# Optimization experiments

Hardware: AMD Instinct MI355X
Metric: run time of the kernel (lower is better)

The kernel has to match this reference:

```python
import jax, jax.numpy as jnp
import numpy as np

B, M, T, L, K = 64, 16, 2048, 64, 32
N = T - L + 1  # 1985 sliding-window positions


def setup_inputs() -> dict:
    key = jax.random.key(0)
    k1, k2, k3 = jax.random.split(key, 3)
    x = jax.random.normal(k1, (B, M, T), dtype=jnp.float32)
    # shapelets initialized uniform(-1, 1) as in nn.init.uniform_
    shapelets = jax.random.uniform(k2, (K, L), dtype=jnp.float32, minval=-1.0, maxval=1.0)
    # penalty maps (learned; zeros at init, random here for a non-trivial weighting)
    penalty_maps = 0.1 * jax.random.normal(k3, (K, M, N), dtype=jnp.float32)
    return {"x": x, "shapelets": shapelets, "penalty_maps": penalty_maps}


def reference(x, shapelets, penalty_maps):
    # x: (B, M, T); shapelets: (K, L); penalty_maps: (K, M, N)
    Lw = shapelets.shape[1]
    n_pos = x.shape[2] - Lw + 1
    # sliding-window view: (B, M, N, L), equivalent to torch unfold(dim=2, size=L, step=1)
    idx = jnp.arange(n_pos)[:, None] + jnp.arange(Lw)[None, :]
    sub = x[:, :, idx]  # (B, M, N, L)

    def per_shapelet(args):
        shp, pmap = args  # (L,), (M, N)
        # raw squared L2 distance over window, per channel/position: (B, M, N)
        raw = jnp.sum((sub - shp[None, None, None, :]) ** 2, axis=3)
        pen = jax.nn.elu(-pmap) + 2.0  # (M, N)
        wd = jnp.sum(raw * pen[None], axis=1)  # sum over channels -> (B, N)
        return jnp.min(wd, axis=1)  # min over positions -> (B,)

    # sequential map over the K shapelets avoids a Kx blow-up of the (B,M,N,L) intermediate
    feats = jax.lax.map(per_shapelet, (shapelets, penalty_maps))  # (K, B)
    return feats.T  # (B, K)
```

## Files before the change

kernel.cpp:

```cpp
#include <hip/hip_runtime.h>
#include <hip/hip_bf16.h>

#define B_ 64
#define M_ 16
#define T_ 2048
#define L_ 64
#define K_ 32
#define N_ (T_ - L_ + 1)
#define TN 64
#define NB 2
#define NTH 256
#define XROW 128
#define STSTR 72
#define SQSTR 68

typedef __attribute__((ext_vector_type(8))) short bf16x8;
typedef __attribute__((ext_vector_type(4))) float f32x4;

__device__ __forceinline__ unsigned short f2bf(float f) {
    __hip_bfloat16 h = __float2bfloat16(f);
    return __builtin_bit_cast(unsigned short, h);
}

__device__ __forceinline__ unsigned funnel16(unsigned lo, unsigned hi, unsigned sh) {
    return (unsigned)(((((unsigned long long)hi) << 32) | lo) >> sh);
}

__device__ __forceinline__ bf16x8 extract_frag(uint4 a, uint4 b, unsigned sh, int c2) {
    unsigned t0 = funnel16(a.x, a.y, sh), t1 = funnel16(a.y, a.z, sh);
    unsigned t2 = funnel16(a.z, a.w, sh), t3 = funnel16(a.w, b.x, sh);
    unsigned t4 = funnel16(b.x, b.y, sh), t5 = funnel16(b.y, b.z, sh);
    unsigned t6 = funnel16(b.z, b.w, sh);
    const bool s2 = (c2 & 2), s1 = (c2 & 1);
    unsigned u0 = s2 ? t2 : t0, u1 = s2 ? t3 : t1, u2 = s2 ? t4 : t2;
    unsigned u3 = s2 ? t5 : t3, u4 = s2 ? t6 : t4;
    union { unsigned u[4]; bf16x8 v; } cvt;
    cvt.u[0] = s1 ? u1 : u0; cvt.u[1] = s1 ? u2 : u1;
    cvt.u[2] = s1 ? u3 : u2; cvt.u[3] = s1 ? u4 : u3;
    return cvt.v;
}

__global__ void init_out_kernel(unsigned* __restrict__ out) {
    int i = blockIdx.x * 256 + threadIdx.x;
    if (i < B_ * K_) out[i] = 0x7F800000u;
}

__global__ __launch_bounds__(NTH, 2)
void shapelet_mfma_kernel(const float* __restrict__ x,
                          const float* __restrict__ shp,
                          const float* __restrict__ pmap,
                          unsigned* __restrict__ out) {
    __shared__ __align__(16) unsigned short xbuf[NB][M_][XROW];
    __shared__ __align__(16) unsigned short st[K_][STSTR];
    __shared__ __align__(16) float sqw[NB][M_][SQSTR];
    __shared__ float ss_l[K_];

    const int tid = threadIdx.x;
    const int n0 = blockIdx.x * TN;
    const int b0 = blockIdx.y * NB;
    const bool fast = (n0 + TN < T_);

    for (int g = tid; g < NB * M_ * 32; g += NTH) {
        const int bi = g >> 9, m = (g >> 5) & 15, j4 = (g & 31) * 4;
        const float* src = x + ((size_t)(b0 + bi) * M_ + m) * T_ + n0 + j4;
        float4 v;
        if (fast) {
            v = *(const float4*)src;
        } else {
            v = make_float4(0.f, 0.f, 0.f, 0.f);
            const int t = n0 + j4;
            if (t     < T_) v.x = src[0];
            if (t + 1 < T_) v.y = src[1];
            if (t + 2 < T_) v.z = src[2];
            if (t + 3 < T_) v.w = src[3];
        }
        ushort4 sv = { f2bf(v.x), f2bf(v.y), f2bf(v.z), f2bf(v.w) };
        *(ushort4*)&xbuf[bi][m][j4] = sv;
    }
    for (int i = tid; i < K_ * 16; i += NTH) {
        const int k = i >> 4, l4 = (i & 15) * 4;
        float4 v = *(const float4*)(shp + k * L_ + l4);
        ushort4 sv = { f2bf(v.x), f2bf(v.y), f2bf(v.z), f2bf(v.w) };
        *(ushort4*)&st[k][l4] = sv;
    }
    if (tid < K_) {
        float s = 0.f;
        for (int l = 0; l < L_; ++l) { float v = shp[tid * L_ + l]; s = fmaf(v, v, s); }
        ss_l[tid] = s;
    }
    {
        const int pm = tid >> 3, th = tid & 7;
        const int bi = pm >> 4, m = pm & 15, j0 = th * 8;
        const float* xr = x + ((size_t)(b0 + bi) * M_ + m) * T_ + n0;
        float s = 0.f;
        if (fast) {
#pragma unroll
            for (int qd = 0; qd < 16; ++qd) {
                float4 v = *(const float4*)(xr + j0 + qd * 4);
                s = fmaf(v.x, v.x, s); s = fmaf(v.y, v.y, s);
                s = fmaf(v.z, v.z, s); s = fmaf(v.w, v.w, s);
            }
            sqw[bi][m][j0] = s;
#pragma unroll
            for (int d = 1; d < 8; ++d) {
                float a = xr[j0 + d + L_ - 1], r = xr[j0 + d - 1];
                s += a * a - r * r;
                sqw[bi][m][j0 + d] = s;
            }
        } else {
            for (int l = 0; l < L_; ++l) {
                float v = (n0 + j0 + l < T_) ? xr[j0 + l] : 0.f;
                s = fmaf(v, v, s);
            }
            sqw[bi][m][j0] = s;
            for (int d = 1; d < 8; ++d) {
                float a = (n0 + j0 + d + L_ - 1 < T_) ? xr[j0 + d + L_ - 1] : 0.f;
                float r = (n0 + j0 + d - 1 < T_) ? xr[j0 + d - 1] : 0.f;
                s += a * a - r * r;
                sqw[bi][m][j0 + d] = s;
            }
        }
    }
    __syncthreads();

    const int lane = tid & 63;
    const int w  = tid >> 6;
    const int rl = lane & 15;
    const int q  = lane >> 4;
    const int rho = rl & 7, r8 = rl >> 3;
    const unsigned sh = (unsigned)((rho & 1) * 16);
    const int c2 = rho >> 1;
    const int Gb = 2 * w + q + r8;

    bf16x8 bfr[2][2];
#pragma unroll
    for (int t = 0; t < 2; ++t)
#pragma unroll
        for (int h = 0; h < 2; ++h)
            bfr[t][h] = *(const bf16x8*)&st[16 * t + rl][8 * q + 32 * h];

    const float ssk0 = ss_l[rl], ssk1 = ss_l[16 + rl];

    f32x4 wd[NB][2];
#pragma unroll
    for (int bi = 0; bi < NB; ++bi) { wd[bi][0] = (f32x4)0.f; wd[bi][1] = (f32x4)0.f; }

    const int nrow = n0 + 16 * w + 4 * q;
    const f32x4 zero = (f32x4)0.f;

#pragma unroll 1
    for (int m = 0; m < M_; ++m) {
        float4 p0, p1;
        const float* pr0 = pmap + ((size_t)(rl * M_ + m)) * N_ + nrow;
        const float* pr1 = pmap + ((size_t)((16 + rl) * M_ + m)) * N_ + nrow;
        if (fast) {
            p0 = *(const float4*)pr0;
            p1 = *(const float4*)pr1;
        } else {
            p0 = make_float4(0.f, 0.f, 0.f, 0.f);
            p1 = make_float4(0.f, 0.f, 0.f, 0.f);
            if (nrow     < N_) { p0.x = pr0[0]; p1.x = pr1[0]; }
            if (nrow + 1 < N_) { p0.y = pr0[1]; p1.y = pr1[1]; }
            if (nrow + 2 < N_) { p0.z = pr0[2]; p1.z = pr1[2]; }
            if (nrow + 3 < N_) { p0.w = pr0[3]; p1.w = pr1[3]; }
        }
        float pen0[4], pen1[4];
        pen0[0] = (p0.x < 0.f) ? (2.f - p0.x) : (__expf(-p0.x) + 1.f);
        pen0[1] = (p0.y < 0.f) ? (2.f - p0.y) : (__expf(-p0.y) + 1.f);
        pen0[2] = (p0.z < 0.f) ? (2.f - p0.z) : (__expf(-p0.z) + 1.f);
        pen0[3] = (p0.w < 0.f) ? (2.f - p0.w) : (__expf(-p0.w) + 1.f);
        pen1[0] = (p1.x < 0.f) ? (2.f - p1.x) : (__expf(-p1.x) + 1.f);
        pen1[1] = (p1.y < 0.f) ? (2.f - p1.y) : (__expf(-p1.y) + 1.f);
        pen1[2] = (p1.z < 0.f) ? (2.f - p1.z) : (__expf(-p1.z) + 1.f);
        pen1[3] = (p1.w < 0.f) ? (2.f - p1.w) : (__expf(-p1.w) + 1.f);

#pragma unroll
        for (int bi = 0; bi < NB; ++bi) {
            const uint4* px = (const uint4*)&xbuf[bi][m][0];
            uint4 w0 = px[Gb],     w1 = px[Gb + 1];
            uint4 w2 = px[Gb + 4], w3 = px[Gb + 5];
            bf16x8 a0 = extract_frag(w0, w1, sh, c2);
            bf16x8 a1 = extract_frag(w2, w3, sh, c2);

            f32x4 corr0 = __builtin_amdgcn_mfma_f32_16x16x32_bf16(a0, bfr[0][0], zero, 0, 0, 0);
            corr0       = __builtin_amdgcn_mfma_f32_16x16x32_bf16(a1, bfr[0][1], corr0, 0, 0, 0);
            f32x4 corr1 = __builtin_amdgcn_mfma_f32_16x16x32_bf16(a0, bfr[1][0], zero, 0, 0, 0);
            corr1       = __builtin_amdgcn_mfma_f32_16x16x32_bf16(a1, bfr[1][1], corr1, 0, 0, 0);

            f32x4 sq = *(const f32x4*)&sqw[bi][m][16 * w + 4 * q];
#pragma unroll
            for (int r = 0; r < 4; ++r) {
                float t0v = fmaf(-2.f, corr0[r], sq[r] + ssk0);
                wd[bi][0][r] = fmaf(pen0[r], t0v, wd[bi][0][r]);
                float t1v = fmaf(-2.f, corr1[r], sq[r] + ssk1);
                wd[bi][1][r] = fmaf(pen1[r], t1v, wd[bi][1][r]);
            }
        }
    }

#pragma unroll
    for (int bi = 0; bi < NB; ++bi) {
#pragma unroll
        for (int t = 0; t < 2; ++t) {
            float lmin = __int_as_float(0x7F800000);
#pragma unroll
            for (int r = 0; r < 4; ++r) {
                if (nrow + r < N_) lmin = fminf(lmin, wd[bi][t][r]);
            }
            lmin = fminf(lmin, __shfl_xor(lmin, 16));
            lmin = fminf(lmin, __shfl_xor(lmin, 32));
            if (q == 0) {
                atomicMin(out + (size_t)(b0 + bi) * K_ + 16 * t + rl,
                          __float_as_uint(fmaxf(lmin, 0.f)));
            }
        }
    }
}

extern "C" void kernel_launch(void* const* d_in, const int* in_sizes, int n_in,
                              void* d_out, int out_size, void* d_ws, size_t ws_size,
                              hipStream_t stream) {
    const float* x    = (const float*)d_in[0];
    const float* shp  = (const float*)d_in[1];
    const float* pmap = (const float*)d_in[2];
    unsigned* out = (unsigned*)d_out;

    init_out_kernel<<<dim3((B_ * K_ + 255) / 256), dim3(256), 0, stream>>>(out);

    dim3 grid((N_ + TN - 1) / TN, B_ / NB);
    shapelet_mfma_kernel<<<grid, dim3(NTH), 0, stream>>>(x, shp, pmap, out);
}
```

Measured before the change: 110.6 us.

## Precompute penalty map in a prepass and process one batch per block

```diff
diff --git a/kernel.cpp b/kernel.cpp
--- a/kernel.cpp
+++ b/kernel.cpp
@@ -7,8 +7,8 @@
 #define L_ 64
 #define K_ 32
 #define N_ (T_ - L_ + 1)
+#define KMN (K_ * M_ * N_)
 #define TN 64
-#define NB 2
 #define NTH 256
 #define XROW 128
 #define STSTR 72
@@ -40,29 +40,42 @@
     return cvt.v;
 }
 
-__global__ void init_out_kernel(unsigned* __restrict__ out) {
-    int i = blockIdx.x * 256 + threadIdx.x;
-    if (i < B_ * K_) out[i] = 0x7F800000u;
+__global__ void pen_init_kernel(const float* __restrict__ pmap,
+                                float* __restrict__ pen,
+                                unsigned* __restrict__ out) {
+    const int gid = blockIdx.x * 256 + threadIdx.x;
+    if (gid < B_ * K_) out[gid] = 0x7F800000u;
+    if (gid < KMN / 4) {
+        const int i4 = gid * 4;
+        float4 p = *(const float4*)(pmap + i4);
+        float4 r;
+        r.x = (p.x < 0.f) ? (2.f - p.x) : (__expf(-p.x) + 1.f);
+        r.y = (p.y < 0.f) ? (2.f - p.y) : (__expf(-p.y) + 1.f);
+        r.z = (p.z < 0.f) ? (2.f - p.z) : (__expf(-p.z) + 1.f);
+        r.w = (p.w < 0.f) ? (2.f - p.w) : (__expf(-p.w) + 1.f);
+        *(float4*)(pen + i4) = r;
+    }
 }
 
 __global__ __launch_bounds__(NTH, 2)
 void shapelet_mfma_kernel(const float* __restrict__ x,
                           const float* __restrict__ shp,
-                          const float* __restrict__ pmap,
+                          const float* __restrict__ pen,
                           unsigned* __restrict__ out) {
-    __shared__ __align__(16) unsigned short xbuf[NB][M_][XROW];
+    __shared__ __align__(16) unsigned short xbuf[M_][XROW];
     __shared__ __align__(16) unsigned short st[K_][STSTR];
-    __shared__ __align__(16) float sqw[NB][M_][SQSTR];
+    __shared__ __align__(16) float sqw[M_][SQSTR];
     __shared__ float ss_l[K_];
 
     const int tid = threadIdx.x;
     const int n0 = blockIdx.x * TN;
-    const int b0 = blockIdx.y * NB;
+    const int b  = blockIdx.y;
     const bool fast = (n0 + TN < T_);
 
-    for (int g = tid; g < NB * M_ * 32; g += NTH) {
-        const int bi = g >> 9, m = (g >> 5) & 15, j4 = (g & 31) * 4;
-        const float* src = x + ((size_t)(b0 + bi) * M_ + m) * T_ + n0 + j4;
+    const float* xb = x + ((size_t)b * M_) * T_ + n0;
+    for (int g = tid; g < M_ * 32; g += NTH) {
+        const int m = g >> 5, j4 = (g & 31) * 4;
+        const float* src = xb + m * T_ + j4;
         float4 v;
         if (fast) {
             v = *(const float4*)src;
@@ -75,7 +88,7 @@
             if (t + 3 < T_) v.w = src[3];
         }
         ushort4 sv = { f2bf(v.x), f2bf(v.y), f2bf(v.z), f2bf(v.w) };
-        *(ushort4*)&xbuf[bi][m][j4] = sv;
+        *(ushort4*)&xbuf[m][j4] = sv;
     }
     for (int i = tid; i < K_ * 16; i += NTH) {
         const int k = i >> 4, l4 = (i & 15) * 4;
@@ -88,10 +101,9 @@
         for (int l = 0; l < L_; ++l) { float v = shp[tid * L_ + l]; s = fmaf(v, v, s); }
         ss_l[tid] = s;
     }
-    {
-        const int pm = tid >> 3, th = tid & 7;
-        const int bi = pm >> 4, m = pm & 15, j0 = th * 8;
-        const float* xr = x + ((size_t)(b0 + bi) * M_ + m) * T_ + n0;
+    if (tid < M_ * 8) {
+        const int m = tid >> 3, j0 = (tid & 7) * 8;
+        const float* xr = x + ((size_t)b * M_ + m) * T_ + n0;
         float s = 0.f;
         if (fast) {
 #pragma unroll
@@ -100,24 +112,24 @@
                 s = fmaf(v.x, v.x, s); s = fmaf(v.y, v.y, s);
                 s = fmaf(v.z, v.z, s); s = fmaf(v.w, v.w, s);
             }
-            sqw[bi][m][j0] = s;
+            sqw[m][j0] = s;
 #pragma unroll
             for (int d = 1; d < 8; ++d) {
                 float a = xr[j0 + d + L_ - 1], r = xr[j0 + d - 1];
                 s += a * a - r * r;
-                sqw[bi][m][j0 + d] = s;
+                sqw[m][j0 + d] = s;
             }
         } else {
             for (int l = 0; l < L_; ++l) {
                 float v = (n0 + j0 + l < T_) ? xr[j0 + l] : 0.f;
                 s = fmaf(v, v, s);
             }
-            sqw[bi][m][j0] = s;
+            sqw[m][j0] = s;
             for (int d = 1; d < 8; ++d) {
                 float a = (n0 + j0 + d + L_ - 1 < T_) ? xr[j0 + d + L_ - 1] : 0.f;
                 float r = (n0 + j0 + d - 1 < T_) ? xr[j0 + d - 1] : 0.f;
                 s += a * a - r * r;
-                sqw[bi][m][j0 + d] = s;
+                sqw[m][j0 + d] = s;
             }
         }
     }
@@ -141,78 +153,63 @@
 
     const float ssk0 = ss_l[rl], ssk1 = ss_l[16 + rl];
 
-    f32x4 wd[NB][2];
-#pragma unroll
-    for (int bi = 0; bi < NB; ++bi) { wd[bi][0] = (f32x4)0.f; wd[bi][1] = (f32x4)0.f; }
-
+    f32x4 wd0 = (f32x4)0.f, wd1 = (f32x4)0.f;
     const int nrow = n0 + 16 * w + 4 * q;
     const f32x4 zero = (f32x4)0.f;
 
-#pragma unroll 1
+#pragma unroll 2
     for (int m = 0; m < M_; ++m) {
         float4 p0, p1;
-        const float* pr0 = pmap + ((size_t)(rl * M_ + m)) * N_ + nrow;
-        const float* pr1 = pmap + ((size_t)((16 + rl) * M_ + m)) * N_ + nrow;
+        const float* pr0 = pen + ((size_t)(rl * M_ + m)) * N_ + nrow;
+        const float* pr1 = pen + ((size_t)((16 + rl) * M_ + m)) * N_ + nrow;
         if (fast) {
             p0 = *(const float4*)pr0;
             p1 = *(const float4*)pr1;
         } else {
-            p0 = make_float4(0.f, 0.f, 0.f, 0.f);
-            p1 = make_float4(0.f, 0.f, 0.f, 0.f);
+            p0 = make_float4(2.f, 2.f, 2.f, 2.f);
+            p1 = make_float4(2.f, 2.f, 2.f, 2.f);
             if (nrow     < N_) { p0.x = pr0[0]; p1.x = pr1[0]; }
             if (nrow + 1 < N_) { p0.y = pr0[1]; p1.y = pr1[1]; }
             if (nrow + 2 < N_) { p0.z = pr0[2]; p1.z = pr1[2]; }
             if (nrow + 3 < N_) { p0.w = pr0[3]; p1.w = pr1[3]; }
         }
-        float pen0[4], pen1[4];
-        pen0[0] = (p0.x < 0.f) ? (2.f - p0.x) : (__expf(-p0.x) + 1.f);
-        pen0[1] = (p0.y < 0.f) ? (2.f - p0.y) : (__expf(-p0.y) + 1.f);
-        pen0[2] = (p0.z < 0.f) ? (2.f - p0.z) : (__expf(-p0.z) + 1.f);
-        pen0[3] = (p0.w < 0.f) ? (2.f - p0.w) : (__expf(-p0.w) + 1.f);
-        pen1[0] = (p1.x < 0.f) ? (2.f - p1.x) : (__expf(-p1.x) + 1.f);
-        pen1[1] = (p1.y < 0.f) ? (2.f - p1.y) : (__expf(-p1.y) + 1.f);
-        pen1[2] = (p1.z < 0.f) ? (2.f - p1.z) : (__expf(-p1.z) + 1.f);
-        pen1[3] = (p1.w < 0.f) ? (2.f - p1.w) : (__expf(-p1.w) + 1.f);
-
-#pragma unroll
-        for (int bi = 0; bi < NB; ++bi) {
-            const uint4* px = (const uint4*)&xbuf[bi][m][0];
-            uint4 w0 = px[Gb],     w1 = px[Gb + 1];
-            uint4 w2 = px[Gb + 4], w3 = px[Gb + 5];
-            bf16x8 a0 = extract_frag(w0, w1, sh, c2);
-            bf16x8 a1 = extract_frag(w2, w3, sh, c2);
-
-            f32x4 corr0 = __builtin_amdgcn_mfma_f32_16x16x32_bf16(a0, bfr[0][0], zero, 0, 0, 0);
-            corr0       = __builtin_amdgcn_mfma_f32_16x16x32_bf16(a1, bfr[0][1], corr0, 0, 0, 0);
-            f32x4 corr1 = __builtin_amdgcn_mfma_f32_16x16x32_bf16(a0, bfr[1][0], zero, 0, 0, 0);
-            corr1       = __builtin_amdgcn_mfma_f32_16x16x32_bf16(a1, bfr[1][1], corr1, 0, 0, 0);
-
-            f32x4 sq = *(const f32x4*)&sqw[bi][m][16 * w + 4 * q];
-#pragma unroll
-            for (int r = 0; r < 4; ++r) {
-                float t0v = fmaf(-2.f, corr0[r], sq[r] + ssk0);
-                wd[bi][0][r] = fmaf(pen0[r], t0v, wd[bi][0][r]);
-                float t1v = fmaf(-2.f, corr1[r], sq[r] + ssk1);
-                wd[bi][1][r] = fmaf(pen1[r], t1v, wd[bi][1][r]);
-            }
-        }
-    }
-
-#pragma unroll
-    for (int bi = 0; bi < NB; ++bi) {
-#pragma unroll
-        for (int t = 0; t < 2; ++t) {
-            float lmin = __int_as_float(0x7F800000);
-#pragma unroll
-            for (int r = 0; r < 4; ++r) {
-                if (nrow + r < N_) lmin = fminf(lmin, wd[bi][t][r]);
-            }
-            lmin = fminf(lmin, __shfl_xor(lmin, 16));
-            lmin = fminf(lmin, __shfl_xor(lmin, 32));
-            if (q == 0) {
-                atomicMin(out + (size_t)(b0 + bi) * K_ + 16 * t + rl,
-                          __float_as_uint(fmaxf(lmin, 0.f)));
-            }
+
+        const uint4* px = (const uint4*)&xbuf[m][0];
+        uint4 w0 = px[Gb],     w1 = px[Gb + 1];
+        uint4 w2 = px[Gb + 4], w3 = px[Gb + 5];
+        bf16x8 a0 = extract_frag(w0, w1, sh, c2);
+        bf16x8 a1 = extract_frag(w2, w3, sh, c2);
+
+        f32x4 corr0 = __builtin_amdgcn_mfma_f32_16x16x32_bf16(a0, bfr[0][0], zero, 0, 0, 0);
+        corr0       = __builtin_amdgcn_mfma_f32_16x16x32_bf16(a1, bfr[0][1], corr0, 0, 0, 0);
+        f32x4 corr1 = __builtin_amdgcn_mfma_f32_16x16x32_bf16(a0, bfr[1][0], zero, 0, 0, 0);
+        corr1       = __builtin_amdgcn_mfma_f32_16x16x32_bf16(a1, bfr[1][1], corr1, 0, 0, 0);
+
+        f32x4 sq = *(const f32x4*)&sqw[m][16 * w + 4 * q];
+        const float pe0[4] = { p0.x, p0.y, p0.z, p0.w };
+        const float pe1[4] = { p1.x, p1.y, p1.z, p1.w };
+#pragma unroll
+        for (int r = 0; r < 4; ++r) {
+            float t0v = fmaf(-2.f, corr0[r], sq[r] + ssk0);
+            wd0[r] = fmaf(pe0[r], t0v, wd0[r]);
+            float t1v = fmaf(-2.f, corr1[r], sq[r] + ssk1);
+            wd1[r] = fmaf(pe1[r], t1v, wd1[r]);
+        }
+    }
+
+#pragma unroll
+    for (int t = 0; t < 2; ++t) {
+        float lmin = __int_as_float(0x7F800000);
+        const f32x4& wdv = t ? wd1 : wd0;
+#pragma unroll
+        for (int r = 0; r < 4; ++r) {
+            if (nrow + r < N_) lmin = fminf(lmin, wdv[r]);
+        }
+        lmin = fminf(lmin, __shfl_xor(lmin, 16));
+        lmin = fminf(lmin, __shfl_xor(lmin, 32));
+        if (q == 0) {
+            atomicMin(out + (size_t)b * K_ + 16 * t + rl,
+                      __float_as_uint(fmaxf(lmin, 0.f)));
         }
     }
 }
@@ -224,9 +221,10 @@
     const float* shp  = (const float*)d_in[1];
     const float* pmap = (const float*)d_in[2];
     unsigned* out = (unsigned*)d_out;
-
-    init_out_kernel<<<dim3((B_ * K_ + 255) / 256), dim3(256), 0, stream>>>(out);
-
-    dim3 grid((N_ + TN - 1) / TN, B_ / NB);
-    shapelet_mfma_kernel<<<grid, dim3(NTH), 0, stream>>>(x, shp, pmap, out);
-}
+    float* pen = (float*)d_ws;
+
+    pen_init_kernel<<<dim3((KMN / 4 + 255) / 256), dim3(256), 0, stream>>>(pmap, pen, out);
+
+    dim3 grid((N_ + TN - 1) / TN, B_);
+    shapelet_mfma_kernel<<<grid, dim3(NTH), 0, stream>>>(x, shp, pen, out);
+}
```

Result: faster. 106.0 us (-4.2%).

## Precompute penalty maps as fp16 in a prepass and halve position tile

Applied to the files above, without the earlier changes.

```diff
diff --git a/kernel.cpp b/kernel.cpp
--- a/kernel.cpp
+++ b/kernel.cpp
@@ -1,4 +1,5 @@
 #include <hip/hip_runtime.h>
+#include <hip/hip_fp16.h>
 #include <hip/hip_bf16.h>
 
 #define B_ 64
@@ -7,12 +8,13 @@
 #define L_ 64
 #define K_ 32
 #define N_ (T_ - L_ + 1)
-#define TN 64
+#define NP 1988
+#define TN 32
 #define NB 2
 #define NTH 256
-#define XROW 128
+#define XROW 96
 #define STSTR 72
-#define SQSTR 68
+#define SQSTR 36
 
 typedef __attribute__((ext_vector_type(8))) short bf16x8;
 typedef __attribute__((ext_vector_type(4))) float f32x4;
@@ -20,6 +22,9 @@
 __device__ __forceinline__ unsigned short f2bf(float f) {
     __hip_bfloat16 h = __float2bfloat16(f);
     return __builtin_bit_cast(unsigned short, h);
+}
+__device__ __forceinline__ float h2f(unsigned short u) {
+    return __half2float(__builtin_bit_cast(__half, u));
 }
 
 __device__ __forceinline__ unsigned funnel16(unsigned lo, unsigned hi, unsigned sh) {
@@ -40,28 +45,54 @@
     return cvt.v;
 }
 
-__global__ void init_out_kernel(unsigned* __restrict__ out) {
-    int i = blockIdx.x * 256 + threadIdx.x;
-    if (i < B_ * K_) out[i] = 0x7F800000u;
+__global__ void pen_init_kernel(const float* __restrict__ pmap,
+                                const float* __restrict__ shp,
+                                unsigned short* __restrict__ penh,
+                                float* __restrict__ ss_ws,
+                                unsigned* __restrict__ out) {
+    const int gid = blockIdx.x * 256 + threadIdx.x;
+    if (gid < B_ * K_) out[gid] = 0x7F800000u;
+    if (gid < K_) {
+        float s = 0.f;
+        for (int l = 0; l < L_; ++l) { float v = shp[gid * L_ + l]; s = fmaf(v, v, s); }
+        ss_ws[gid] = s;
+    }
+    const int RQ = NP / 4;
+    if (gid < K_ * M_ * RQ) {
+        const int r = gid / RQ;
+        const int q4 = (gid - r * RQ) * 4;
+        const float* src = pmap + (size_t)r * N_;
+        ushort4 o;
+        unsigned short* po = (unsigned short*)&o;
+#pragma unroll
+        for (int i = 0; i < 4; ++i) {
+            int n = q4 + i; if (n >= N_) n = N_ - 1;
+            const float p = src[n];
+            const float pe = (p < 0.f) ? (2.f - p) : (__expf(-p) + 1.f);
+            po[i] = __builtin_bit_cast(unsigned short, __float2half(pe));
+        }
+        *(ushort4*)(penh + (size_t)r * NP + q4) = o;
+    }
 }
 
 __global__ __launch_bounds__(NTH, 2)
 void shapelet_mfma_kernel(const float* __restrict__ x,
                           const float* __restrict__ shp,
-                          const float* __restrict__ pmap,
+                          const unsigned short* __restrict__ penh,
+                          const float* __restrict__ ss_ws,
                           unsigned* __restrict__ out) {
     __shared__ __align__(16) unsigned short xbuf[NB][M_][XROW];
     __shared__ __align__(16) unsigned short st[K_][STSTR];
     __shared__ __align__(16) float sqw[NB][M_][SQSTR];
-    __shared__ float ss_l[K_];
 
     const int tid = threadIdx.x;
     const int n0 = blockIdx.x * TN;
     const int b0 = blockIdx.y * NB;
-    const bool fast = (n0 + TN < T_);
-
-    for (int g = tid; g < NB * M_ * 32; g += NTH) {
-        const int bi = g >> 9, m = (g >> 5) & 15, j4 = (g & 31) * 4;
+    const bool fast = (n0 + XROW <= T_);
+
+    for (int g = tid; g < NB * M_ * 24; g += NTH) {
+        const int bi = g / 384, rem = g - bi * 384;
+        const int m = rem / 24, j4 = (rem - m * 24) * 4;
         const float* src = x + ((size_t)(b0 + bi) * M_ + m) * T_ + n0 + j4;
         float4 v;
         if (fast) {
@@ -83,14 +114,8 @@
         ushort4 sv = { f2bf(v.x), f2bf(v.y), f2bf(v.z), f2bf(v.w) };
         *(ushort4*)&st[k][l4] = sv;
     }
-    if (tid < K_) {
-        float s = 0.f;
-        for (int l = 0; l < L_; ++l) { float v = shp[tid * L_ + l]; s = fmaf(v, v, s); }
-        ss_l[tid] = s;
-    }
-    {
-        const int pm = tid >> 3, th = tid & 7;
-        const int bi = pm >> 4, m = pm & 15, j0 = th * 8;
+    if (tid < NB * M_ * 4) {
+        const int bi = tid >> 6, m = (tid >> 2) & 15, j0 = (tid & 3) * 8;
         const float* xr = x + ((size_t)(b0 + bi) * M_ + m) * T_ + n0;
         float s = 0.f;
         if (fast) {
@@ -124,13 +149,16 @@
     __syncthreads();
 
     const int lane = tid & 63;
-    const int w  = tid >> 6;
+    const int w    = tid >> 6;
+    const int bi   = w >> 1;
+    const int nsub = w & 1;
     const int rl = lane & 15;
     const int q  = lane >> 4;
     const int rho = rl & 7, r8 = rl >> 3;
     const unsigned sh = (unsigned)((rho & 1) * 16);
     const int c2 = rho >> 1;
-    const int Gb = 2 * w + q + r8;
+    const int Gb = 2 * nsub + q + r8;
+    const int nrow = n0 + 16 * nsub + 4 * q;
 
     bf16x8 bfr[2][2];
 #pragma unroll
@@ -139,80 +167,67 @@
         for (int h = 0; h < 2; ++h)
             bfr[t][h] = *(const bf16x8*)&st[16 * t + rl][8 * q + 32 * h];
 
-    const float ssk0 = ss_l[rl], ssk1 = ss_l[16 + rl];
-
-    f32x4 wd[NB][2];
-#pragma unroll
-    for (int bi = 0; bi < NB; ++bi) { wd[bi][0] = (f32x4)0.f; wd[bi][1] = (f32x4)0.f; }
-
-    const int nrow = n0 + 16 * w + 4 * q;
+    const float ssk0 = ss_ws[rl], ssk1 = ss_ws[16 + rl];
+
+    const unsigned short* ph0 = penh + (size_t)rl * (M_ * NP) + nrow;
+    const unsigned short* ph1 = ph0 + (size_t)16 * M_ * NP;
+
+    f32x4 wd0 = (f32x4)0.f, wd1 = (f32x4)0.f;
     const f32x4 zero = (f32x4)0.f;
 
-#pragma unroll 1
+#pragma unroll 2
     for (int m = 0; m < M_; ++m) {
-        float4 p0, p1;
-        const float* pr0 = pmap + ((size_t)(rl * M_ + m)) * N_ + nrow;
-        const float* pr1 = pmap + ((size_t)((16 + rl) * M_ + m)) * N_ + nrow;
+        float pe0[4], pe1[4];
         if (fast) {
-            p0 = *(const float4*)pr0;
-            p1 = *(const float4*)pr1;
+            ushort4 h0 = *(const ushort4*)(ph0 + (size_t)m * NP);
+            ushort4 h1 = *(const ushort4*)(ph1 + (size_t)m * NP);
+            pe0[0] = h2f(h0.x); pe0[1] = h2f(h0.y); pe0[2] = h2f(h0.z); pe0[3] = h2f(h0.w);
+            pe1[0] = h2f(h1.x); pe1[1] = h2f(h1.y); pe1[2] = h2f(h1.z); pe1[3] = h2f(h1.w);
         } else {
-            p0 = make_float4(0.f, 0.f, 0.f, 0.f);
-            p1 = make_float4(0.f, 0.f, 0.f, 0.f);
-            if (nrow     < N_) { p0.x = pr0[0]; p1.x = pr1[0]; }
-            if (nrow + 1 < N_) { p0.y = pr0[1]; p1.y = pr1[1]; }
-            if (nrow + 2 < N_) { p0.z = pr0[2]; p1.z = pr1[2]; }
-            if (nrow + 3 < N_) { p0.w = pr0[3]; p1.w = pr1[3]; }
-        }
-        float pen0[4], pen1[4];
-        pen0[0] = (p0.x < 0.f) ? (2.f - p0.x) : (__expf(-p0.x) + 1.f);
-        pen0[1] = (p0.y < 0.f) ? (2.f - p0.y) : (__expf(-p0.y) + 1.f);
-        pen0[2] = (p0.z < 0.f) ? (2.f - p0.z) : (__expf(-p0.z) + 1.f);
-        pen0[3] = (p0.w < 0.f) ? (2.f - p0.w) : (__expf(-p0.w) + 1.f);
-        pen1[0] = (p1.x < 0.f) ? (2.f - p1.x) : (__expf(-p1.x) + 1.f);
-        pen1[1] = (p1.y < 0.f) ? (2.f - p1.y) : (__expf(-p1.y) + 1.f);
-        pen1[2] = (p1.z < 0.f) ? (2.f - p1.z) : (__expf(-p1.z) + 1.f);
-        pen1[3] = (p1.w < 0.f) ? (2.f - p1.w) : (__expf(-p1.w) + 1.f);
-
-#pragma unroll
-        for (int bi = 0; bi < NB; ++bi) {
-            const uint4* px = (const uint4*)&xbuf[bi][m][0];
-            uint4 w0 = px[Gb],     w1 = px[Gb + 1];
-            uint4 w2 = px[Gb + 4], w3 = px[Gb + 5];
-            bf16x8 a0 = extract_frag(w0, w1, sh, c2);
-            bf16x8 a1 = extract_frag(w2, w3, sh, c2);
-
-            f32x4 corr0 = __builtin_amdgcn_mfma_f32_16x16x32_bf16(a0, bfr[0][0], zero, 0, 0, 0);
-            corr0       = __builtin_amdgcn_mfma_f32_16x16x32_bf16(a1, bfr[0][1], corr0, 0, 0, 0);
-            f32x4 corr1 = __builtin_amdgcn_mfma_f32_16x16x32_bf16(a0, bfr[1][0], zero, 0, 0, 0);
-            corr1       = __builtin_amdgcn_mfma_f32_16x16x32_bf16(a1, bfr[1][1], corr1, 0, 0, 0);
-
-            f32x4 sq = *(const f32x4*)&sqw[bi][m][16 * w + 4 * q];
-#pragma unroll
-            for (int r = 0; r < 4; ++r) {
-                float t0v = fmaf(-2.f, corr0[r], sq[r] + ssk0);
-                wd[bi][0][r] = fmaf(pen0[r], t0v, wd[bi][0][r]);
-                float t1v = fmaf(-2.f, corr1[r], sq[r] + ssk1);
-                wd[bi][1][r] = fmaf(pen1[r], t1v, wd[bi][1][r]);
-            }
-        }
-    }
-
-#pragma unroll
-    for (int bi = 0; bi < NB; ++bi) {
-#pragma unroll
-        for (int t = 0; t < 2; ++t) {
-            float lmin = __int_as_float(0x7F800000);
-#pragma unroll
-            for (int r = 0; r < 4; ++r) {
-                if (nrow + r < N_) lmin = fminf(lmin, wd[bi][t][r]);
-            }
-            lmin = fminf(lmin, __shfl_xor(lmin, 16));
-            lmin = fminf(lmin, __shfl_xor(lmin, 32));
-            if (q == 0) {
-                atomicMin(out + (size_t)(b0 + bi) * K_ + 16 * t + rl,
-                          __float_as_uint(fmaxf(lmin, 0.f)));
-            }
+            const unsigned short* r0_ = ph0 + (size_t)m * NP;
+            const unsigned short* r1_ = ph1 + (size_t)m * NP;
+#pragma unroll
+            for (int i = 0; i < 4; ++i) {
+                const bool valid = (nrow + i) < N_;
+                pe0[i] = valid ? h2f(r0_[i]) : 2.f;
+                pe1[i] = valid ? h2f(r1_[i]) : 2.f;
+            }
+        }
+
+        const uint4* px = (const uint4*)&xbuf[bi][m][0];
+        uint4 w0_ = px[Gb],     w1_ = px[Gb + 1];
+        uint4 w2_ = px[Gb + 4], w3_ = px[Gb + 5];
+        bf16x8 a0 = extract_frag(w0_, w1_, sh, c2);
+        bf16x8 a1 = extract_frag(w2_, w3_, sh, c2);
+
+        f32x4 c0_ = __builtin_amdgcn_mfma_f32_16x16x32_bf16(a0, bfr[0][0], zero, 0, 0, 0);
+        c0_       = __builtin_amdgcn_mfma_f32_16x16x32_bf16(a1, bfr[0][1], c0_, 0, 0, 0);
+        f32x4 c1_ = __builtin_amdgcn_mfma_f32_16x16x32_bf16(a0, bfr[1][0], zero, 0, 0, 0);
+        c1_       = __builtin_amdgcn_mfma_f32_16x16x32_bf16(a1, bfr[1][1], c1_, 0, 0, 0);
+
+        f32x4 sq = *(const f32x4*)&sqw[bi][m][16 * nsub + 4 * q];
+#pragma unroll
+        for (int r = 0; r < 4; ++r) {
+            float t0v = fmaf(-2.f, c0_[r], sq[r] + ssk0);
+            wd0[r] = fmaf(pe0[r], t0v, wd0[r]);
+            float t1v = fmaf(-2.f, c1_[r], sq[r] + ssk1);
+            wd1[r] = fmaf(pe1[r], t1v, wd1[r]);
+        }
+    }
+
+#pragma unroll
+    for (int t = 0; t < 2; ++t) {
+        float lmin = __int_as_float(0x7F800000);
+        const f32x4& wdv = t ? wd1 : wd0;
+#pragma unroll
+        for (int r = 0; r < 4; ++r) {
+            if (nrow + r < N_) lmin = fminf(lmin, wdv[r]);
+        }
+        lmin = fminf(lmin, __shfl_xor(lmin, 16));
+        lmin = fminf(lmin, __shfl_xor(lmin, 32));
+        if (q == 0) {
+            atomicMin(out + (size_t)(b0 + bi) * K_ + 16 * t + rl,
+                      __float_as_uint(fmaxf(lmin, 0.f)));
         }
     }
 }
@@ -224,9 +239,13 @@
     const float* shp  = (const float*)d_in[1];
     const float* pmap = (const float*)d_in[2];
     unsigned* out = (unsigned*)d_out;
-
-    init_out_kernel<<<dim3((B_ * K_ + 255) / 256), dim3(256), 0, stream>>>(out);
+    unsigned short* penh = (unsigned short*)d_ws;
+    float* ss_ws = (float*)(penh + (size_t)K_ * M_ * NP);
+
+    const int work = K_ * M_ * (NP / 4);
+    pen_init_kernel<<<dim3((work + 255) / 256), dim3(256), 0, stream>>>(
+        pmap, shp, penh, ss_ws, out);
 
     dim3 grid((N_ + TN - 1) / TN, B_ / NB);
-    shapelet_mfma_kernel<<<grid, dim3(NTH), 0, stream>>>(x, shp, pmap, out);
-}
+    shapelet_mfma_kernel<<<grid, dim3(NTH), 0, stream>>>(x, shp, penh, ss_ws, out);
+}
```

Result: slower. 113.9 us (+3.0%).
